# Performance work log

Measured on AMD Instinct MI355X. Metric: run time of the kernel, lower is better.

Reference implementation:

```python
import jax, jax.numpy as jnp
import numpy as np

H = 1024        # hidden_size
NH = 16         # num_attention_heads
DH = H // NH    # head dim = 64
I = 4096        # intermediate_size
E = 8           # moe_num_experts
B, S = 2, 2048
EPS = 1e-12


def _ln(x, g, b):
    mu = jnp.mean(x, axis=-1, keepdims=True)
    var = jnp.mean(jnp.square(x - mu), axis=-1, keepdims=True)
    return (x - mu) * jax.lax.rsqrt(var + EPS) * g + b


def setup_inputs() -> dict:
    key = jax.random.key(0)
    ks = jax.random.split(key, 16)
    std = 0.02
    p = {
        "hidden_states": jax.random.normal(ks[0], (B, S, H), jnp.float32),
        "Wq": jax.random.normal(ks[1], (H, H), jnp.float32) * std,
        "bq": jnp.zeros((H,), jnp.float32),
        "Wk": jax.random.normal(ks[2], (H, H), jnp.float32) * std,
        "bk": jnp.zeros((H,), jnp.float32),
        "Wv": jax.random.normal(ks[3], (H, H), jnp.float32) * std,
        "bv": jnp.zeros((H,), jnp.float32),
        "Wao": jax.random.normal(ks[4], (H, H), jnp.float32) * std,
        "bao": jnp.zeros((H,), jnp.float32),
        "ln1_g": jnp.ones((H,), jnp.float32),
        "ln1_b": jnp.zeros((H,), jnp.float32),
        "router_w": jax.random.normal(ks[5], (H, E), jnp.float32) * std,
        "We": jax.random.normal(ks[6], (E, H, I), jnp.float32) * std,
        "be": jnp.zeros((E, I), jnp.float32),
        "Wo": jax.random.normal(ks[7], (I, H), jnp.float32) * std,
        "bo": jnp.zeros((H,), jnp.float32),
        "ln2_g": jnp.ones((H,), jnp.float32),
        "ln2_b": jnp.zeros((H,), jnp.float32),
    }
    return p


def reference(hidden_states, Wq, bq, Wk, bk, Wv, bv, Wao, bao, ln1_g, ln1_b,
              router_w, We, be, Wo, bo, ln2_g, ln2_b):
    x = hidden_states  # [B,S,H]

    def heads(t):  # [B,S,H] -> [B,NH,S,DH]
        return t.reshape(B, S, NH, DH).transpose(0, 2, 1, 3)

    q = heads(x @ Wq + bq)
    k = heads(x @ Wk + bk)
    v = heads(x @ Wv + bv)
    scores = jnp.einsum("bhqd,bhkd->bhqk", q, k) / jnp.sqrt(jnp.float32(DH))
    probs = jax.nn.softmax(scores, axis=-1)
    ctx = jnp.einsum("bhqk,bhkd->bhqd", probs, v)
    ctx = ctx.transpose(0, 2, 1, 3).reshape(B, S, H)
    attn_out = _ln(ctx @ Wao + bao + x, ln1_g, ln1_b)  # BertSelfOutput

    # ---- MoE FFN: top-1 routing, per-expert GELU MLP, shared output proj ----
    flat = attn_out.reshape(-1, H)              # [N,H]
    logits = flat @ router_w                    # [N,E]
    idx = jnp.argmax(logits, axis=-1)           # top-1 of softmax == argmax of logits
    inter = jnp.zeros((flat.shape[0], I), flat.dtype)
    for e in range(E):  # small fixed expert count
        h_e = jax.nn.gelu(flat @ We[e] + be[e], approximate=False)
        inter = jnp.where((idx == e)[:, None], h_e, inter)
    inter = inter.reshape(B, S, I)
    out = _ln(inter @ Wo + bo + attn_out, ln2_g, ln2_b)  # BertOutput
    return out
```

## Files before the change

### kernel.cpp

```cpp
#include <hip/hip_runtime.h>
#include <hip/hip_bf16.h>
#include <cstdint>

#define H_  1024
#define NH_ 16
#define DH_ 64
#define I_  4096
#define E_  8
#define B_  2
#define S_  2048
#define N_  4096
#define QKVLD 3072
#define LN_EPS 1e-12f

typedef __attribute__((ext_vector_type(4))) float f4;
typedef __attribute__((ext_vector_type(8))) short s8v;
typedef unsigned int u32;

__device__ __forceinline__ float bf2f(unsigned short u) {
  union { unsigned int i; float f; } c; c.i = ((unsigned int)u) << 16; return c.f;
}
__device__ __forceinline__ unsigned short f2bf(float f) {
  __hip_bfloat16 h = __float2bfloat16(f);
  return *reinterpret_cast<unsigned short*>(&h);
}
__device__ __forceinline__ u32 pack_bf2(float a, float b) {
  return (u32)f2bf(a) | ((u32)f2bf(b) << 16);
}
__device__ __forceinline__ float gelu_f(float x) {
  return 0.5f * x * (1.0f + erff(x * 0.70710678118f));
}
__device__ __forceinline__ void gload16(const void* g, void* l) {
  __builtin_amdgcn_global_load_lds(
      (const __attribute__((address_space(1))) void*)g,
      (__attribute__((address_space(3))) void*)l, 16, 0, 0);
}

__global__ __launch_bounds__(256) void cvt_bf16_kernel(
    const float* __restrict__ in, ushort* __restrict__ out, int n8)
{
  const int t = blockIdx.x * 256 + threadIdx.x;
  if (t >= n8) return;
  const f4 x0 = *(const f4*)(in + (size_t)t * 8);
  const f4 x1 = *(const f4*)(in + (size_t)t * 8 + 4);
  s8v o;
#pragma unroll
  for (int j = 0; j < 4; ++j) { o[j] = (short)f2bf(x0[j]); o[4 + j] = (short)f2bf(x1[j]); }
  *(s8v*)(out + (size_t)t * 8) = o;
}

__global__ __launch_bounds__(256) void transpose_cvt_kernel(
    const float* __restrict__ in, ushort* __restrict__ out, int R, int C)
{
  __shared__ float Ls[64][68];
  const size_t zo = (size_t)blockIdx.z * (size_t)R * C;
  const int bx = blockIdx.x << 6;
  const int by = blockIdx.y << 6;
  const int tid = threadIdx.x;
  const int lr = tid >> 4, lc4 = (tid & 15) << 2;
  const float* ip = in + zo + (size_t)(by + lr) * C + bx + lc4;
#pragma unroll
  for (int i = 0; i < 4; ++i)
    *(f4*)&Ls[lr + (i << 4)][lc4] = *(const f4*)(ip + (size_t)(i << 4) * C);
  __syncthreads();
  const int oc = tid >> 2, seg = (tid & 3) << 4;
  ushort* op = out + zo + (size_t)(bx + oc) * R + by + seg;
  s8v v0, v1;
#pragma unroll
  for (int j = 0; j < 8; ++j) {
    v0[j] = (short)f2bf(Ls[seg + j][oc]);
    v1[j] = (short)f2bf(Ls[seg + 8 + j][oc]);
  }
  *(s8v*)op = v0;
  *(s8v*)(op + 8) = v1;
}

__global__ void concat3_kernel(const float* a, const float* b, const float* c,
                               float* __restrict__ o)
{
  const int t = blockIdx.x * 256 + threadIdx.x;
  if (t < 1024) o[t] = a[t];
  else if (t < 2048) o[t] = b[t - 1024];
  else o[t] = c[t - 2048];
}

__global__ __launch_bounds__(256) void gather_kernel(
    const ushort* __restrict__ X, const int* __restrict__ lists,
    ushort* __restrict__ Xg)
{
  const int r = (blockIdx.x << 1) + (threadIdx.x >> 7);
  const int c = (threadIdx.x & 127) << 3;
  const int tok = lists[r];
  *(s8v*)&Xg[(size_t)r * H_ + c] = *(const s8v*)&X[(size_t)tok * H_ + c];
}

__global__ __launch_bounds__(512, 2) void gemm256_bf16_kernel(
    const ushort* __restrict__ A, const ushort* __restrict__ Bt,
    const float* __restrict__ bias, ushort* __restrict__ Cout,
    const int M, const int N, const int K)
{
  __shared__ __align__(16) ushort Asm[2][4][256][8];
  __shared__ __align__(16) ushort Bsm[2][4][256][8];
  const int tid = threadIdx.x, w = tid >> 6, l = tid & 63;
  const int lq = l & 15, g = l >> 4;
  const int wm = w >> 2, wn = w & 3;
  const int nbx = N >> 8;
  const int nwg = nbx * (M >> 8);
  int id = blockIdx.y * nbx + blockIdx.x;
  id = (id & 7) * (nwg >> 3) + (id >> 3);
  const int m0 = (id / nbx) << 8, n0 = (id % nbx) << 8;

  const bool isB = (w >= 4);
  const int ks = w & 3;
  const ushort* gb = isB ? (Bt + (size_t)(n0 + l) * K + (ks << 3))
                         : (A + (size_t)(m0 + l) * K + (ks << 3));
  const ushort* p0 = gb;
  const ushort* p1 = gb + (size_t)64 * K;
  const ushort* p2 = gb + (size_t)128 * K;
  const ushort* p3 = gb + (size_t)192 * K;

  f4 acc[8][4] = {};
  const int nt = K >> 5;
#define STG(tt, buf) { const int kt_ = (tt) << 5;                          \
    ushort* d = isB ? &Bsm[buf][ks][0][0] : &Asm[buf][ks][0][0];           \
    gload16(p0 + kt_, d);          gload16(p1 + kt_, d + 64 * 8);          \
    gload16(p2 + kt_, d + 128 * 8); gload16(p3 + kt_, d + 192 * 8); }
  STG(0, 0);
  STG(1, 1);
  for (int t = 0; t < nt; ++t) {
    const int cur = t & 1;
    if (t + 1 < nt) { asm volatile("s_waitcnt vmcnt(4)" ::: "memory"); }
    else            { asm volatile("s_waitcnt vmcnt(0)" ::: "memory"); }
    __builtin_amdgcn_s_barrier();
    __builtin_amdgcn_sched_barrier(0);
    s8v af[8], bfv[4];
#pragma unroll
    for (int mi = 0; mi < 8; ++mi)
      af[mi] = *(const s8v*)&Asm[cur][g][(wm << 7) + (mi << 4) + lq][0];
#pragma unroll
    for (int ni = 0; ni < 4; ++ni)
      bfv[ni] = *(const s8v*)&Bsm[cur][g][(wn << 6) + (ni << 4) + lq][0];
    asm volatile("s_waitcnt lgkmcnt(0)" ::: "memory");
    __builtin_amdgcn_sched_barrier(0);
    __builtin_amdgcn_s_barrier();
    __builtin_amdgcn_sched_barrier(0);
    if (t + 2 < nt) STG(t + 2, cur);
#pragma unroll
    for (int mi = 0; mi < 8; ++mi)
#pragma unroll
      for (int ni = 0; ni < 4; ++ni)
        acc[mi][ni] = __builtin_amdgcn_mfma_f32_16x16x32_bf16(af[mi], bfv[ni], acc[mi][ni], 0, 0, 0);
  }
#undef STG
  __syncthreads();
  ushort* st = (ushort*)Asm + (size_t)w * (16 * 72);
  float bs[4];
#pragma unroll
  for (int ni = 0; ni < 4; ++ni) bs[ni] = bias[n0 + (wn << 6) + (ni << 4) + lq];
#pragma unroll
  for (int mi = 0; mi < 8; ++mi) {
#pragma unroll
    for (int ni = 0; ni < 4; ++ni)
#pragma unroll
      for (int r = 0; r < 4; ++r)
        st[((g << 2) + r) * 72 + (ni << 4) + lq] = f2bf(acc[mi][ni][r] + bs[ni]);
#pragma unroll
    for (int q2 = 0; q2 < 2; ++q2) {
      const int r16 = l & 15, ch = (l >> 4) + (q2 << 2);
      const s8v vv = *(const s8v*)&st[r16 * 72 + (ch << 3)];
      *(s8v*)&Cout[(size_t)(m0 + (wm << 7) + (mi << 4) + r16) * N
                   + n0 + (wn << 6) + (ch << 3)] = vv;
    }
  }
}

__global__ __launch_bounds__(512, 2) void moe256_mfma_kernel(
    const ushort* __restrict__ Xg, const ushort* __restrict__ WeT,
    const float* __restrict__ be, const int* __restrict__ lists,
    const int* __restrict__ offs, const int* __restrict__ cnt,
    const int* __restrict__ tb, ushort* __restrict__ inter)
{
  __shared__ __align__(16) ushort Asm[2][4][256][8];
  __shared__ __align__(16) ushort Bsm[2][4][256][8];
  __shared__ int tokL[256];
  const int by = blockIdx.y;
  if (by >= tb[E_]) return;
  int e = 0;
#pragma unroll
  for (int t = 1; t < E_; ++t) if (by >= tb[t]) e = t;
  const int rt = by - tb[e];
  const int base = offs[e] + (rt << 8);
  const int nrows = cnt[e] - (rt << 8);
  const int tid = threadIdx.x;
  if (tid < 256) tokL[tid] = (tid < nrows) ? lists[base + tid] : -1;
  __syncthreads();
  const int w = tid >> 6, l = tid & 63;
  const int lq = l & 15, g = l >> 4;
  const int wm = w >> 2, wn = w & 3;
  const int n0 = blockIdx.x << 8;

  const bool isB = (w >= 4);
  const int ks = w & 3;
  const ushort* Wp = WeT + (size_t)e * I_ * H_;
  const ushort* p0;
  const ushort* p1;
  const ushort* p2;
  const ushort* p3;
  if (isB) {
    const ushort* gb = Wp + (size_t)(n0 + l) * H_ + (ks << 3);
    p0 = gb; p1 = gb + (size_t)64 * H_; p2 = gb + (size_t)128 * H_; p3 = gb + (size_t)192 * H_;
  } else {
    p0 = Xg + (size_t)min(base + l,       N_ - 1) * H_ + (ks << 3);
    p1 = Xg + (size_t)min(base + 64 + l,  N_ - 1) * H_ + (ks << 3);
    p2 = Xg + (size_t)min(base + 128 + l, N_ - 1) * H_ + (ks << 3);
    p3 = Xg + (size_t)min(base + 192 + l, N_ - 1) * H_ + (ks << 3);
  }

  f4 acc[8][4] = {};
#define STG(tt, buf) { const int kt_ = (tt) << 5;                          \
    ushort* d = isB ? &Bsm[buf][ks][0][0] : &Asm[buf][ks][0][0];           \
    gload16(p0 + kt_, d);          gload16(p1 + kt_, d + 64 * 8);          \
    gload16(p2 + kt_, d + 128 * 8); gload16(p3 + kt_, d + 192 * 8); }
  STG(0, 0);
  STG(1, 1);
  for (int t = 0; t < 32; ++t) {
    const int cur = t & 1;
    if (t + 1 < 32) { asm volatile("s_waitcnt vmcnt(4)" ::: "memory"); }
    else            { asm volatile("s_waitcnt vmcnt(0)" ::: "memory"); }
    __builtin_amdgcn_s_barrier();
    __builtin_amdgcn_sched_barrier(0);
    s8v af[8], bfv[4];
#pragma unroll
    for (int mi = 0; mi < 8; ++mi)
      af[mi] = *(const s8v*)&Asm[cur][g][(wm << 7) + (mi << 4) + lq][0];
#pragma unroll
    for (int ni = 0; ni < 4; ++ni)
      bfv[ni] = *(const s8v*)&Bsm[cur][g][(wn << 6) + (ni << 4) + lq][0];
    asm volatile("s_waitcnt lgkmcnt(0)" ::: "memory");
    __builtin_amdgcn_sched_barrier(0);
    __builtin_amdgcn_s_barrier();
    __builtin_amdgcn_sched_barrier(0);
    if (t + 2 < 32) STG(t + 2, cur);
#pragma unroll
    for (int mi = 0; mi < 8; ++mi)
#pragma unroll
      for (int ni = 0; ni < 4; ++ni)
        acc[mi][ni] = __builtin_amdgcn_mfma_f32_16x16x32_bf16(af[mi], bfv[ni], acc[mi][ni], 0, 0, 0);
  }
#undef STG
  __syncthreads();
  ushort* st = (ushort*)Asm + (size_t)w * (16 * 72);
  float bs[4];
#pragma unroll
  for (int ni = 0; ni < 4; ++ni)
    bs[ni] = be[(size_t)e * I_ + n0 + (wn << 6) + (ni << 4) + lq];
#pragma unroll
  for (int mi = 0; mi < 8; ++mi) {
#pragma unroll
    for (int ni = 0; ni < 4; ++ni)
#pragma unroll
      for (int r = 0; r < 4; ++r)
        st[((g << 2) + r) * 72 + (ni << 4) + lq] = f2bf(gelu_f(acc[mi][ni][r] + bs[ni]));
#pragma unroll
    for (int q2 = 0; q2 < 2; ++q2) {
      const int r16 = l & 15, ch = (l >> 4) + (q2 << 2);
      const int tok = tokL[(wm << 7) + (mi << 4) + r16];
      if (tok >= 0) {
        const s8v vv = *(const s8v*)&st[r16 * 72 + (ch << 3)];
        *(s8v*)&inter[(size_t)tok * I_ + n0 + (wn << 6) + (ch << 3)] = vv;
      }
    }
  }
}

template <bool BF16OUT, int KSPLIT>
__global__ __launch_bounds__(256, 3) void gemm_mfma_kernel(
    const ushort* __restrict__ A, const ushort* __restrict__ Bt,
    const float* __restrict__ bias, void* __restrict__ Cout,
    const int M, const int N, const int K)
{
  __shared__ __align__(16) ushort Asm[3][4][128][8];
  __shared__ __align__(16) ushort Bsm[3][4][128][8];
  const int tid = threadIdx.x;
  const int w = tid >> 6, l = tid & 63;
  const int lq = l & 15, g = l >> 4;
  const int wm = w >> 1, wn = w & 1;
  const int nbx = N >> 7;
  const int nwg = nbx * (M >> 7);
  int id = blockIdx.y * nbx + blockIdx.x;
  id = (id & 7) * (nwg >> 3) + (id >> 3);
  const int m0 = (id / nbx) << 7, n0 = (id % nbx) << 7;
  const int Kspan = K / KSPLIT;
  const int kbase = (KSPLIT > 1) ? blockIdx.z * Kspan : 0;

  const ushort* a0 = A + (size_t)(m0 + l) * K + kbase + (w << 3);
  const ushort* a1 = a0 + (size_t)64 * K;
  const ushort* b0 = Bt + (size_t)(n0 + l) * K + kbase + (w << 3);
  const ushort* b1 = b0 + (size_t)64 * K;

  f4 acc[4][4] = {};
  const int nt = Kspan >> 5;
#define STAGE_G(tt, buf)                                   \
  { const int kt_ = (tt) << 5;                             \
    gload16(a0 + kt_, &Asm[buf][w][0][0]);                 \
    gload16(a1 + kt_, &Asm[buf][w][64][0]);                \
    gload16(b0 + kt_, &Bsm[buf][w][0][0]);                 \
    gload16(b1 + kt_, &Bsm[buf][w][64][0]); }
  STAGE_G(0, 0);
  STAGE_G(1, 1);
  int cur = 0, nxt2 = 2;
  for (int t = 0; t < nt; ++t) {
    if (t + 1 < nt) { asm volatile("s_waitcnt vmcnt(4)" ::: "memory"); }
    else            { asm volatile("s_waitcnt vmcnt(0)" ::: "memory"); }
    __builtin_amdgcn_s_barrier();
    __builtin_amdgcn_sched_barrier(0);
    if (t + 2 < nt) STAGE_G(t + 2, nxt2);
    s8v af[4], bfv[4];
#pragma unroll
    for (int mi = 0; mi < 4; ++mi)
      af[mi] = *(const s8v*)&Asm[cur][g][(wm << 6) + (mi << 4) + lq][0];
#pragma unroll
    for (int ni = 0; ni < 4; ++ni)
      bfv[ni] = *(const s8v*)&Bsm[cur][g][(wn << 6) + (ni << 4) + lq][0];
    asm volatile("s_waitcnt lgkmcnt(0)" ::: "memory");
    __builtin_amdgcn_sched_barrier(0);
#pragma unroll
    for (int mi = 0; mi < 4; ++mi)
#pragma unroll
      for (int ni = 0; ni < 4; ++ni)
        acc[mi][ni] = __builtin_amdgcn_mfma_f32_16x16x32_bf16(af[mi], bfv[ni], acc[mi][ni], 0, 0, 0);
    cur = (cur == 2) ? 0 : cur + 1;
    nxt2 = (nxt2 == 2) ? 0 : nxt2 + 1;
  }
#undef STAGE_G
  if constexpr (BF16OUT) {
    __syncthreads();
    ushort* st = (ushort*)Asm + (size_t)w * (16 * 72);
    float bs[4];
#pragma unroll
    for (int ni = 0; ni < 4; ++ni) bs[ni] = bias[n0 + (wn << 6) + (ni << 4) + lq];
#pragma unroll
    for (int mi = 0; mi < 4; ++mi) {
#pragma unroll
      for (int ni = 0; ni < 4; ++ni)
#pragma unroll
        for (int r = 0; r < 4; ++r)
          st[((g << 2) + r) * 72 + (ni << 4) + lq] = f2bf(acc[mi][ni][r] + bs[ni]);
#pragma unroll
      for (int q2 = 0; q2 < 2; ++q2) {
        const int r16 = l & 15, ch = (l >> 4) + (q2 << 2);
        const s8v vv = *(const s8v*)&st[r16 * 72 + (ch << 3)];
        *(s8v*)&((ushort*)Cout)[(size_t)(m0 + (wm << 6) + (mi << 4) + r16) * N
                                + n0 + (wn << 6) + (ch << 3)] = vv;
      }
    }
  } else {
    float* outf = (float*)Cout + (size_t)blockIdx.z * M * N;
#pragma unroll
    for (int ni = 0; ni < 4; ++ni) {
      const int col = n0 + (wn << 6) + (ni << 4) + lq;
      const float bs = (KSPLIT == 1 || blockIdx.z == 0) ? bias[col] : 0.f;
#pragma unroll
      for (int mi = 0; mi < 4; ++mi) {
        const int row = m0 + (wm << 6) + (mi << 4) + (g << 2);
#pragma unroll
        for (int r = 0; r < 4; ++r)
          outf[(size_t)(row + r) * N + col] = acc[mi][ni][r] + bs;
      }
    }
  }
}

__global__ __launch_bounds__(256) void attn_mfma_kernel(
    const ushort* __restrict__ qkv, ushort* __restrict__ ctx)
{
  __shared__ __align__(16) ushort Ks[64 * 72];
  __shared__ __align__(16) ushort Vr[64 * 72];
  __shared__ __align__(16) ushort Vt[64 * 72];
  __shared__ __align__(16) ushort Ps[4][16 * 72];
  const int bid0 = blockIdx.x;
  const int bid  = ((bid0 & 7) << 7) + (bid0 >> 3);
  const int bh = bid >> 5, qt = bid & 31;
  const int b = bh >> 4, h = bh & 15;
  const int tid = threadIdx.x, w = tid >> 6, l = tid & 63;
  const int lq = l & 15, g = l >> 4;
  const size_t bS = (size_t)b * S_;
  const ushort* qb = qkv + bS * QKVLD + h * DH_;
  const ushort* kb = qb + 1024;
  const ushort* vb = qb + 2048;

  s8v qf0, qf1;
  {
    const ushort* qp = qb + (size_t)(qt * 64 + w * 16 + lq) * QKVLD;
    qf0 = *(const s8v*)(qp + (g << 3));
    qf1 = *(const s8v*)(qp + 32 + (g << 3));
  }

  f4 o0 = {0,0,0,0}, o1 = {0,0,0,0}, o2 = {0,0,0,0}, o3 = {0,0,0,0};
  float mrun = -3.0e38f, lrun = 0.f;

  const int skey = tid >> 2;
  const int sd   = (tid & 3) << 4;

  s8v kr0, kr1, vr0, vr1;
#define ALOAD(t_) {                                                        \
    const ushort* kp_ = kb + (size_t)((t_) * 64 + skey) * QKVLD + sd;      \
    kr0 = *(const s8v*)kp_; kr1 = *(const s8v*)(kp_ + 8);                  \
    const ushort* vp_ = vb + (size_t)((t_) * 64 + skey) * QKVLD + sd;      \
    vr0 = *(const s8v*)vp_; vr1 = *(const s8v*)(vp_ + 8); }
#define AWRITE() {                                                         \
    *(s8v*)&Ks[skey * 72 + sd]     = kr0;                                  \
    *(s8v*)&Ks[skey * 72 + sd + 8] = kr1;                                  \
    *(s8v*)&Vr[skey * 72 + sd]     = vr0;                                  \
    *(s8v*)&Vr[skey * 72 + sd + 8] = vr1; }

  ALOAD(0); AWRITE();
  ALOAD(1);

  for (int kt = 0; kt < 32; ++kt) {
    asm volatile("s_waitcnt lgkmcnt(0)" ::: "memory");
    __builtin_amdgcn_sched_barrier(0);
    __builtin_amdgcn_s_barrier();
    __builtin_amdgcn_sched_barrier(0);

    {
      s8v t0, t1;
#pragma unroll
      for (int j = 0; j < 8; ++j) {
        t0[j] = (short)Vr[(w * 16 + j) * 72 + l];
        t1[j] = (short)Vr[(w * 16 + 8 + j) * 72 + l];
      }
      *(s8v*)&Vt[l * 72 + w * 16]     = t0;
      *(s8v*)&Vt[l * 72 + w * 16 + 8] = t1;
    }

    float s[16];
    __builtin_amdgcn_s_setprio(1);
#pragma unroll
    for (int st = 0; st < 4; ++st) {
      f4 acc = {0, 0, 0, 0};
      const s8v ka0 = *(const s8v*)&Ks[(st * 16 + lq) * 72 + (g << 3)];
      const s8v ka1 = *(const s8v*)&Ks[(st * 16 + lq) * 72 + 32 + (g << 3)];
      acc = __builtin_amdgcn_mfma_f32_16x16x32_bf16(ka0, qf0, acc, 0, 0, 0);
      acc = __builtin_amdgcn_mfma_f32_16x16x32_bf16(ka1, qf1, acc, 0, 0, 0);
      s[st * 4 + 0] = acc[0] * 0.125f; s[st * 4 + 1] = acc[1] * 0.125f;
      s[st * 4 + 2] = acc[2] * 0.125f; s[st * 4 + 3] = acc[3] * 0.125f;
    }
    __builtin_amdgcn_s_setprio(0);

    float tmax = s[0];
#pragma unroll
    for (int i = 1; i < 16; ++i) tmax = fmaxf(tmax, s[i]);
    tmax = fmaxf(tmax, __shfl_xor(tmax, 16));
    tmax = fmaxf(tmax, __shfl_xor(tmax, 32));
    if (!__all(tmax - mrun <= 8.f)) {
      const float mnew  = fmaxf(mrun, tmax);
      const float alpha = __expf(mrun - mnew);
      f4 av;
      av[0] = __shfl(alpha, g * 4 + 0); av[1] = __shfl(alpha, g * 4 + 1);
      av[2] = __shfl(alpha, g * 4 + 2); av[3] = __shfl(alpha, g * 4 + 3);
      o0 *= av; o1 *= av; o2 *= av; o3 *= av;
      lrun *= alpha; mrun = mnew;
    }
    float psum = 0.f;
#pragma unroll
    for (int i = 0; i < 16; ++i) { s[i] = __expf(s[i] - mrun); psum += s[i]; }
    psum += __shfl_xor(psum, 16); psum += __shfl_xor(psum, 32);
    lrun += psum;

    {
      ushort* pw = &Ps[w][lq * 72];
#pragma unroll
      for (int st = 0; st < 4; ++st) {
        *(u32*)&pw[st * 16 + g * 4 + 0] = pack_bf2(s[st * 4 + 0], s[st * 4 + 1]);
        *(u32*)&pw[st * 16 + g * 4 + 2] = pack_bf2(s[st * 4 + 2], s[st * 4 + 3]);
      }
    }
    asm volatile("s_waitcnt lgkmcnt(0)" ::: "memory");
    __builtin_amdgcn_sched_barrier(0);
    __builtin_amdgcn_s_barrier();
    __builtin_amdgcn_sched_barrier(0);

    __builtin_amdgcn_s_setprio(1);
#pragma unroll
    for (int ks = 0; ks < 2; ++ks) {
      const int kof = ks * 32 + (g << 3);
      const s8v pa = *(const s8v*)&Ps[w][lq * 72 + kof];
      const s8v v0 = *(const s8v*)&Vt[( 0 + lq) * 72 + kof];
      const s8v v1 = *(const s8v*)&Vt[(16 + lq) * 72 + kof];
      const s8v v2 = *(const s8v*)&Vt[(32 + lq) * 72 + kof];
      const s8v v3 = *(const s8v*)&Vt[(48 + lq) * 72 + kof];
      o0 = __builtin_amdgcn_mfma_f32_16x16x32_bf16(pa, v0, o0, 0, 0, 0);
      o1 = __builtin_amdgcn_mfma_f32_16x16x32_bf16(pa, v1, o1, 0, 0, 0);
      o2 = __builtin_amdgcn_mfma_f32_16x16x32_bf16(pa, v2, o2, 0, 0, 0);
      o3 = __builtin_amdgcn_mfma_f32_16x16x32_bf16(pa, v3, o3, 0, 0, 0);
    }
    __builtin_amdgcn_s_setprio(0);

    if (kt + 1 < 32) AWRITE();
    if (kt + 2 < 32) ALOAD(kt + 2);
  }
#undef ALOAD
#undef AWRITE

  const float inv = 1.f / lrun;
#pragma unroll
  for (int r = 0; r < 4; ++r) {
    const float li = __shfl(inv, g * 4 + r);
    ushort* op = ctx + (bS + (size_t)(qt * 64 + w * 16 + g * 4 + r)) * H_ + h * DH_ + lq;
    op[0]  = f2bf(o0[r] * li);
    op[16] = f2bf(o1[r] * li);
    op[32] = f2bf(o2[r] * li);
    op[48] = f2bf(o3[r] * li);
  }
}

template <int P>
__global__ __launch_bounds__(256) void add_ln_kernel(
    const float* __restrict__ a, const float* __restrict__ r,
    const float* __restrict__ g, const float* __restrict__ bta,
    float* __restrict__ out, ushort* __restrict__ ob)
{
  const int row = blockIdx.x, tid = threadIdx.x;
  const size_t base = (size_t)row * H_;
  const float4 xr = *(const float4*)(r + base + (tid << 2));
  float4 x = xr;
#pragma unroll
  for (int pp = 0; pp < P; ++pp) {
    const float4 xa = *(const float4*)(a + (size_t)pp * N_ * H_ + base + (tid << 2));
    x.x += xa.x; x.y += xa.y; x.z += xa.z; x.w += xa.w;
  }
  float s  = x.x + x.y + x.z + x.w;
  float ss = x.x * x.x + x.y * x.y + x.z * x.z + x.w * x.w;
#pragma unroll
  for (int off = 1; off < 64; off <<= 1) { s += __shfl_xor(s, off); ss += __shfl_xor(ss, off); }
  __shared__ float red[8];
  const int w = tid >> 6, ln = tid & 63;
  if (ln == 0) { red[w] = s; red[4 + w] = ss; }
  __syncthreads();
  const float S  = red[0] + red[1] + red[2] + red[3];
  const float SS = red[4] + red[5] + red[6] + red[7];
  const float mu  = S * (1.f / 1024.f);
  const float var = fmaxf(SS * (1.f / 1024.f) - mu * mu, 0.f);
  const float inv = rsqrtf(var + LN_EPS);
  const float4 gg = *(const float4*)&g[tid << 2];
  const float4 bb = *(const float4*)&bta[tid << 2];
  float4 y;
  y.x = (x.x - mu) * inv * gg.x + bb.x;
  y.y = (x.y - mu) * inv * gg.y + bb.y;
  y.z = (x.z - mu) * inv * gg.z + bb.z;
  y.w = (x.w - mu) * inv * gg.w + bb.w;
  *(float4*)&out[base + (tid << 2)] = y;
  if (ob) {
    ushort4 u;
    u.x = f2bf(y.x); u.y = f2bf(y.y); u.z = f2bf(y.z); u.w = f2bf(y.w);
    *(ushort4*)&ob[base + (tid << 2)] = u;
  }
}

__global__ __launch_bounds__(64) void router_kernel(
    const float* __restrict__ x, const float* __restrict__ rw,
    int* __restrict__ idx, int* __restrict__ cnt)
{
  const int t = blockIdx.x, lane = threadIdx.x;
  float acc[8] = {0.f};
  for (int c = 0; c < H_; c += 64) {
    const float xv = x[(size_t)t * H_ + c + lane];
    const float* wr = rw + (size_t)(c + lane) * E_;
    const float4 w0 = *(const float4*)wr;
    const float4 w1 = *(const float4*)(wr + 4);
    acc[0] += xv * w0.x; acc[1] += xv * w0.y; acc[2] += xv * w0.z; acc[3] += xv * w0.w;
    acc[4] += xv * w1.x; acc[5] += xv * w1.y; acc[6] += xv * w1.z; acc[7] += xv * w1.w;
  }
#pragma unroll
  for (int e = 0; e < E_; ++e) {
    float s = acc[e];
#pragma unroll
    for (int off = 1; off < 64; off <<= 1) s += __shfl_xor(s, off);
    acc[e] = s;
  }
  if (lane == 0) {
    int be_ = 0; float bv = acc[0];
#pragma unroll
    for (int e = 1; e < E_; ++e) if (acc[e] > bv) { bv = acc[e]; be_ = e; }
    idx[t] = be_;
    atomicAdd(&cnt[be_], 1);
  }
}

__global__ void init_kernel(int* cnt) { if (threadIdx.x < E_) cnt[threadIdx.x] = 0; }

__global__ void scan_kernel(const int* __restrict__ cnt, int* __restrict__ offs,
                            int* __restrict__ cursor, int* __restrict__ tb)
{
  int o = 0, tt = 0;
  for (int e = 0; e < E_; ++e) {
    offs[e] = o; cursor[e] = o; tb[e] = tt;
    o += cnt[e]; tt += (cnt[e] + 255) >> 8;
  }
  tb[E_] = tt;
}

__global__ __launch_bounds__(256) void scatter_kernel(
    const int* __restrict__ idx, int* __restrict__ cursor, int* __restrict__ lists)
{
  const int t = blockIdx.x * 256 + threadIdx.x;
  if (t < N_) {
    const int e = idx[t];
    const int p = atomicAdd(&cursor[e], 1);
    lists[p] = t;
  }
}

extern "C" void kernel_launch(void* const* d_in, const int* in_sizes, int n_in,
                              void* d_out, int out_size, void* d_ws, size_t ws_size,
                              hipStream_t stream) {
  const float* x   = (const float*)d_in[0];
  const float* Wq  = (const float*)d_in[1];
  const float* bq  = (const float*)d_in[2];
  const float* Wk  = (const float*)d_in[3];
  const float* bk  = (const float*)d_in[4];
  const float* Wv  = (const float*)d_in[5];
  const float* bv  = (const float*)d_in[6];
  const float* Wao = (const float*)d_in[7];
  const float* bao = (const float*)d_in[8];
  const float* g1  = (const float*)d_in[9];
  const float* b1  = (const float*)d_in[10];
  const float* rw  = (const float*)d_in[11];
  const float* We  = (const float*)d_in[12];
  const float* be  = (const float*)d_in[13];
  const float* Wo  = (const float*)d_in[14];
  const float* bo  = (const float*)d_in[15];
  const float* g2  = (const float*)d_in[16];
  const float* b2  = (const float*)d_in[17];
  float* out = (float*)d_out;

  char* p = (char*)d_ws;
  int* idx    = (int*)p; p += (size_t)N_ * 4;
  int* cnt    = (int*)p; p += 8 * 4;
  int* offs   = (int*)p; p += 8 * 4;
  int* cursor = (int*)p; p += 8 * 4;
  int* tb     = (int*)p; p += 16 * 4;
  int* lists  = (int*)p; p += (size_t)N_ * 4;
  p = (char*)(((uintptr_t)p + 255) & ~(uintptr_t)255);
  const size_t NH = (size_t)N_ * H_;
  ushort* xb     = (ushort*)p; p += NH * 2;
  ushort* qkvb   = (ushort*)p;
  float*  woPart = (float*)p;  p += (size_t)N_ * QKVLD * 2;
  ushort* ctxb   = (ushort*)p; p += NH * 2;
  float*  attn   = (float*)p;  p += NH * 4;
  ushort* attnb  = (ushort*)p; p += NH * 2;
  ushort* interb = (ushort*)p;
  float*  aoPart = (float*)p;  p += (size_t)N_ * I_ * 2;
  ushort* WqkvT  = (ushort*)p; p += (size_t)QKVLD * H_ * 2;
  ushort* WaoT   = (ushort*)p; p += (size_t)H_ * H_ * 2;
  ushort* WoT    = (ushort*)p; p += (size_t)H_ * I_ * 2;
  ushort* WeT    = (ushort*)p; p += (size_t)E_ * I_ * H_ * 2;
  float*  bqkv   = (float*)p;  p += QKVLD * 4;
  ushort* Xg     = xb;

  const dim3 blk(256);

  init_kernel<<<1, 64, 0, stream>>>(cnt);
  cvt_bf16_kernel<<<(N_ * H_ / 8 + 255) / 256, blk, 0, stream>>>(x, xb, N_ * H_ / 8);
  concat3_kernel<<<QKVLD / 256, blk, 0, stream>>>(bq, bk, bv, bqkv);
  transpose_cvt_kernel<<<dim3(16, 16, 1), blk, 0, stream>>>(Wq, WqkvT, H_, H_);
  transpose_cvt_kernel<<<dim3(16, 16, 1), blk, 0, stream>>>(Wk, WqkvT + (size_t)1024 * H_, H_, H_);
  transpose_cvt_kernel<<<dim3(16, 16, 1), blk, 0, stream>>>(Wv, WqkvT + (size_t)2048 * H_, H_, H_);
  transpose_cvt_kernel<<<dim3(16, 16, 1), blk, 0, stream>>>(Wao, WaoT, H_, H_);
  transpose_cvt_kernel<<<dim3(16, 64, 1), blk, 0, stream>>>(Wo, WoT, I_, H_);
  transpose_cvt_kernel<<<dim3(64, 16, 8), blk, 0, stream>>>(We, WeT, H_, I_);

  gemm256_bf16_kernel<<<dim3(QKVLD / 256, N_ / 256), dim3(512), 0, stream>>>(
      xb, WqkvT, bqkv, qkvb, N_, QKVLD, H_);
  attn_mfma_kernel<<<1024, blk, 0, stream>>>(qkvb, ctxb);
  gemm_mfma_kernel<false, 2><<<dim3(H_ / 128, N_ / 128, 2), blk, 0, stream>>>(
      ctxb, WaoT, bao, aoPart, N_, H_, H_);
  add_ln_kernel<2><<<N_, blk, 0, stream>>>(aoPart, x, g1, b1, attn, attnb);
  router_kernel<<<N_, 64, 0, stream>>>(attn, rw, idx, cnt);
  scan_kernel<<<1, 1, 0, stream>>>(cnt, offs, cursor, tb);
  scatter_kernel<<<N_ / 256, blk, 0, stream>>>(idx, cursor, lists);
  gather_kernel<<<N_ / 2, blk, 0, stream>>>(attnb, lists, Xg);
  moe256_mfma_kernel<<<dim3(I_ / 256, N_ / 256 + E_), dim3(512), 0, stream>>>(
      Xg, WeT, be, lists, offs, cnt, tb, interb);
  gemm_mfma_kernel<false, 2><<<dim3(H_ / 128, N_ / 128, 2), blk, 0, stream>>>(
      interb, WoT, bo, woPart, N_, H_, I_);
  add_ln_kernel<2><<<N_, blk, 0, stream>>>(woPart, attn, g2, b2, out, (ushort*)nullptr);
}
```

Baseline: 516.6 us.

## Use 256-tile split-K GEMM for projections and fuse routing scan/scatter

Generalizes the 256x256 tile, 512-thread GEMM with a bf16/fp32 output template and a split-K template, and uses it for the attention-output and FFN-output projections instead of the 128x128 kernel. It also folds the expert-count reset into the input conversion kernel and merges the scan and scatter into one single-block kernel with a shared-memory cursor. The intent is higher per-block data reuse and fewer kernel launches. The trade-off is that the projection GEMMs now launch only 128 blocks, which may leave many compute units idle.

```diff
diff --git a/kernel.cpp b/kernel.cpp
--- a/kernel.cpp
+++ b/kernel.cpp
@@ -37,8 +37,9 @@
 }
 
 __global__ __launch_bounds__(256) void cvt_bf16_kernel(
-    const float* __restrict__ in, ushort* __restrict__ out, int n8)
-{
+    const float* __restrict__ in, ushort* __restrict__ out, int n8, int* __restrict__ cnt)
+{
+  if (blockIdx.x == 0 && threadIdx.x < E_) cnt[threadIdx.x] = 0;
   const int t = blockIdx.x * 256 + threadIdx.x;
   if (t >= n8) return;
   const f4 x0 = *(const f4*)(in + (size_t)t * 8);
@@ -84,6 +85,28 @@
   else o[t] = c[t - 2048];
 }
 
+__global__ __launch_bounds__(256) void scan_scatter_kernel(
+    const int* __restrict__ idx, const int* __restrict__ cnt,
+    int* __restrict__ offs, int* __restrict__ tb, int* __restrict__ lists)
+{
+  __shared__ int lcur[E_];
+  const int tid = threadIdx.x;
+  if (tid == 0) {
+    int o = 0, tt = 0;
+    for (int e = 0; e < E_; ++e) {
+      offs[e] = o; lcur[e] = o; tb[e] = tt;
+      o += cnt[e]; tt += (cnt[e] + 255) >> 8;
+    }
+    tb[E_] = tt;
+  }
+  __syncthreads();
+  for (int t = tid; t < N_; t += 256) {
+    const int e = idx[t];
+    const int p = atomicAdd(&lcur[e], 1);
+    lists[p] = t;
+  }
+}
+
 __global__ __launch_bounds__(256) void gather_kernel(
     const ushort* __restrict__ X, const int* __restrict__ lists,
     ushort* __restrict__ Xg)
@@ -94,9 +117,10 @@
   *(s8v*)&Xg[(size_t)r * H_ + c] = *(const s8v*)&X[(size_t)tok * H_ + c];
 }
 
-__global__ __launch_bounds__(512, 2) void gemm256_bf16_kernel(
+template <bool BF16OUT, int KSPLIT>
+__global__ __launch_bounds__(512, 2) void gemm256_kernel(
     const ushort* __restrict__ A, const ushort* __restrict__ Bt,
-    const float* __restrict__ bias, ushort* __restrict__ Cout,
+    const float* __restrict__ bias, void* __restrict__ Cout,
     const int M, const int N, const int K)
 {
   __shared__ __align__(16) ushort Asm[2][4][256][8];
@@ -109,18 +133,20 @@
   int id = blockIdx.y * nbx + blockIdx.x;
   id = (id & 7) * (nwg >> 3) + (id >> 3);
   const int m0 = (id / nbx) << 8, n0 = (id % nbx) << 8;
+  const int Kspan = K / KSPLIT;
+  const int kbase = (KSPLIT > 1) ? blockIdx.z * Kspan : 0;
 
   const bool isB = (w >= 4);
   const int ks = w & 3;
-  const ushort* gb = isB ? (Bt + (size_t)(n0 + l) * K + (ks << 3))
-                         : (A + (size_t)(m0 + l) * K + (ks << 3));
+  const ushort* gb = isB ? (Bt + (size_t)(n0 + l) * K + kbase + (ks << 3))
+                         : (A + (size_t)(m0 + l) * K + kbase + (ks << 3));
   const ushort* p0 = gb;
   const ushort* p1 = gb + (size_t)64 * K;
   const ushort* p2 = gb + (size_t)128 * K;
   const ushort* p3 = gb + (size_t)192 * K;
 
   f4 acc[8][4] = {};
-  const int nt = K >> 5;
+  const int nt = Kspan >> 5;
 #define STG(tt, buf) { const int kt_ = (tt) << 5;                          \
     ushort* d = isB ? &Bsm[buf][ks][0][0] : &Asm[buf][ks][0][0];           \
     gload16(p0 + kt_, d);          gload16(p1 + kt_, d + 64 * 8);          \
@@ -152,24 +178,40 @@
         acc[mi][ni] = __builtin_amdgcn_mfma_f32_16x16x32_bf16(af[mi], bfv[ni], acc[mi][ni], 0, 0, 0);
   }
 #undef STG
-  __syncthreads();
-  ushort* st = (ushort*)Asm + (size_t)w * (16 * 72);
-  float bs[4];
-#pragma unroll
-  for (int ni = 0; ni < 4; ++ni) bs[ni] = bias[n0 + (wn << 6) + (ni << 4) + lq];
-#pragma unroll
-  for (int mi = 0; mi < 8; ++mi) {
-#pragma unroll
-    for (int ni = 0; ni < 4; ++ni)
-#pragma unroll
-      for (int r = 0; r < 4; ++r)
-        st[((g << 2) + r) * 72 + (ni << 4) + lq] = f2bf(acc[mi][ni][r] + bs[ni]);
-#pragma unroll
-    for (int q2 = 0; q2 < 2; ++q2) {
-      const int r16 = l & 15, ch = (l >> 4) + (q2 << 2);
-      const s8v vv = *(const s8v*)&st[r16 * 72 + (ch << 3)];
-      *(s8v*)&Cout[(size_t)(m0 + (wm << 7) + (mi << 4) + r16) * N
-                   + n0 + (wn << 6) + (ch << 3)] = vv;
+  if constexpr (BF16OUT) {
+    __syncthreads();
+    ushort* st = (ushort*)Asm + (size_t)w * (16 * 72);
+    float bs[4];
+#pragma unroll
+    for (int ni = 0; ni < 4; ++ni) bs[ni] = bias[n0 + (wn << 6) + (ni << 4) + lq];
+#pragma unroll
+    for (int mi = 0; mi < 8; ++mi) {
+#pragma unroll
+      for (int ni = 0; ni < 4; ++ni)
+#pragma unroll
+        for (int r = 0; r < 4; ++r)
+          st[((g << 2) + r) * 72 + (ni << 4) + lq] = f2bf(acc[mi][ni][r] + bs[ni]);
+#pragma unroll
+      for (int q2 = 0; q2 < 2; ++q2) {
+        const int r16 = l & 15, ch = (l >> 4) + (q2 << 2);
+        const s8v vv = *(const s8v*)&st[r16 * 72 + (ch << 3)];
+        *(s8v*)&((ushort*)Cout)[(size_t)(m0 + (wm << 7) + (mi << 4) + r16) * N
+                                + n0 + (wn << 6) + (ch << 3)] = vv;
+      }
+    }
+  } else {
+    float* outf = (float*)Cout + (size_t)blockIdx.z * M * N;
+#pragma unroll
+    for (int ni = 0; ni < 4; ++ni) {
+      const int col = n0 + (wn << 6) + (ni << 4) + lq;
+      const float bs = (KSPLIT == 1 || blockIdx.z == 0) ? bias[col] : 0.f;
+#pragma unroll
+      for (int mi = 0; mi < 8; ++mi) {
+        const int row = m0 + (wm << 7) + (mi << 4) + (g << 2);
+#pragma unroll
+        for (int r = 0; r < 4; ++r)
+          outf[(size_t)(row + r) * N + col] = acc[mi][ni][r] + bs;
+      }
     }
   }
 }
@@ -268,104 +310,6 @@
       if (tok >= 0) {
         const s8v vv = *(const s8v*)&st[r16 * 72 + (ch << 3)];
         *(s8v*)&inter[(size_t)tok * I_ + n0 + (wn << 6) + (ch << 3)] = vv;
-      }
-    }
-  }
-}
-
-template <bool BF16OUT, int KSPLIT>
-__global__ __launch_bounds__(256, 3) void gemm_mfma_kernel(
-    const ushort* __restrict__ A, const ushort* __restrict__ Bt,
-    const float* __restrict__ bias, void* __restrict__ Cout,
-    const int M, const int N, const int K)
-{
-  __shared__ __align__(16) ushort Asm[3][4][128][8];
-  __shared__ __align__(16) ushort Bsm[3][4][128][8];
-  const int tid = threadIdx.x;
-  const int w = tid >> 6, l = tid & 63;
-  const int lq = l & 15, g = l >> 4;
-  const int wm = w >> 1, wn = w & 1;
-  const int nbx = N >> 7;
-  const int nwg = nbx * (M >> 7);
-  int id = blockIdx.y * nbx + blockIdx.x;
-  id = (id & 7) * (nwg >> 3) + (id >> 3);
-  const int m0 = (id / nbx) << 7, n0 = (id % nbx) << 7;
-  const int Kspan = K / KSPLIT;
-  const int kbase = (KSPLIT > 1) ? blockIdx.z * Kspan : 0;
-
-  const ushort* a0 = A + (size_t)(m0 + l) * K + kbase + (w << 3);
-  const ushort* a1 = a0 + (size_t)64 * K;
-  const ushort* b0 = Bt + (size_t)(n0 + l) * K + kbase + (w << 3);
-  const ushort* b1 = b0 + (size_t)64 * K;
-
-  f4 acc[4][4] = {};
-  const int nt = Kspan >> 5;
-#define STAGE_G(tt, buf)                                   \
-  { const int kt_ = (tt) << 5;                             \
-    gload16(a0 + kt_, &Asm[buf][w][0][0]);                 \
-    gload16(a1 + kt_, &Asm[buf][w][64][0]);                \
-    gload16(b0 + kt_, &Bsm[buf][w][0][0]);                 \
-    gload16(b1 + kt_, &Bsm[buf][w][64][0]); }
-  STAGE_G(0, 0);
-  STAGE_G(1, 1);
-  int cur = 0, nxt2 = 2;
-  for (int t = 0; t < nt; ++t) {
-    if (t + 1 < nt) { asm volatile("s_waitcnt vmcnt(4)" ::: "memory"); }
-    else            { asm volatile("s_waitcnt vmcnt(0)" ::: "memory"); }
-    __builtin_amdgcn_s_barrier();
-    __builtin_amdgcn_sched_barrier(0);
-    if (t + 2 < nt) STAGE_G(t + 2, nxt2);
-    s8v af[4], bfv[4];
-#pragma unroll
-    for (int mi = 0; mi < 4; ++mi)
-      af[mi] = *(const s8v*)&Asm[cur][g][(wm << 6) + (mi << 4) + lq][0];
-#pragma unroll
-    for (int ni = 0; ni < 4; ++ni)
-      bfv[ni] = *(const s8v*)&Bsm[cur][g][(wn << 6) + (ni << 4) + lq][0];
-    asm volatile("s_waitcnt lgkmcnt(0)" ::: "memory");
-    __builtin_amdgcn_sched_barrier(0);
-#pragma unroll
-    for (int mi = 0; mi < 4; ++mi)
-#pragma unroll
-      for (int ni = 0; ni < 4; ++ni)
-        acc[mi][ni] = __builtin_amdgcn_mfma_f32_16x16x32_bf16(af[mi], bfv[ni], acc[mi][ni], 0, 0, 0);
-    cur = (cur == 2) ? 0 : cur + 1;
-    nxt2 = (nxt2 == 2) ? 0 : nxt2 + 1;
-  }
-#undef STAGE_G
-  if constexpr (BF16OUT) {
-    __syncthreads();
-    ushort* st = (ushort*)Asm + (size_t)w * (16 * 72);
-    float bs[4];
-#pragma unroll
-    for (int ni = 0; ni < 4; ++ni) bs[ni] = bias[n0 + (wn << 6) + (ni << 4) + lq];
-#pragma unroll
-    for (int mi = 0; mi < 4; ++mi) {
-#pragma unroll
-      for (int ni = 0; ni < 4; ++ni)
-#pragma unroll
-        for (int r = 0; r < 4; ++r)
-          st[((g << 2) + r) * 72 + (ni << 4) + lq] = f2bf(acc[mi][ni][r] + bs[ni]);
-#pragma unroll
-      for (int q2 = 0; q2 < 2; ++q2) {
-        const int r16 = l & 15, ch = (l >> 4) + (q2 << 2);
-        const s8v vv = *(const s8v*)&st[r16 * 72 + (ch << 3)];
-        *(s8v*)&((ushort*)Cout)[(size_t)(m0 + (wm << 6) + (mi << 4) + r16) * N
-                                + n0 + (wn << 6) + (ch << 3)] = vv;
-      }
-    }
-  } else {
-    float* outf = (float*)Cout + (size_t)blockIdx.z * M * N;
-#pragma unroll
-    for (int ni = 0; ni < 4; ++ni) {
-      const int col = n0 + (wn << 6) + (ni << 4) + lq;
-      const float bs = (KSPLIT == 1 || blockIdx.z == 0) ? bias[col] : 0.f;
-#pragma unroll
-      for (int mi = 0; mi < 4; ++mi) {
-        const int row = m0 + (wm << 6) + (mi << 4) + (g << 2);
-#pragma unroll
-        for (int r = 0; r < 4; ++r)
-          outf[(size_t)(row + r) * N + col] = acc[mi][ni][r] + bs;
       }
     }
   }
@@ -588,30 +532,6 @@
   }
 }
 
-__global__ void init_kernel(int* cnt) { if (threadIdx.x < E_) cnt[threadIdx.x] = 0; }
-
-__global__ void scan_kernel(const int* __restrict__ cnt, int* __restrict__ offs,
-                            int* __restrict__ cursor, int* __restrict__ tb)
-{
-  int o = 0, tt = 0;
-  for (int e = 0; e < E_; ++e) {
-    offs[e] = o; cursor[e] = o; tb[e] = tt;
-    o += cnt[e]; tt += (cnt[e] + 255) >> 8;
-  }
-  tb[E_] = tt;
-}
-
-__global__ __launch_bounds__(256) void scatter_kernel(
-    const int* __restrict__ idx, int* __restrict__ cursor, int* __restrict__ lists)
-{
-  const int t = blockIdx.x * 256 + threadIdx.x;
-  if (t < N_) {
-    const int e = idx[t];
-    const int p = atomicAdd(&cursor[e], 1);
-    lists[p] = t;
-  }
-}
-
 extern "C" void kernel_launch(void* const* d_in, const int* in_sizes, int n_in,
                               void* d_out, int out_size, void* d_ws, size_t ws_size,
                               hipStream_t stream) {
@@ -639,7 +559,6 @@
   int* idx    = (int*)p; p += (size_t)N_ * 4;
   int* cnt    = (int*)p; p += 8 * 4;
   int* offs   = (int*)p; p += 8 * 4;
-  int* cursor = (int*)p; p += 8 * 4;
   int* tb     = (int*)p; p += 16 * 4;
   int* lists  = (int*)p; p += (size_t)N_ * 4;
   p = (char*)(((uintptr_t)p + 255) & ~(uintptr_t)255);
@@ -660,9 +579,9 @@
   ushort* Xg     = xb;
 
   const dim3 blk(256);
-
-  init_kernel<<<1, 64, 0, stream>>>(cnt);
-  cvt_bf16_kernel<<<(N_ * H_ / 8 + 255) / 256, blk, 0, stream>>>(x, xb, N_ * H_ / 8);
+  const dim3 blk512(512);
+
+  cvt_bf16_kernel<<<(N_ * H_ / 8 + 255) / 256, blk, 0, stream>>>(x, xb, N_ * H_ / 8, cnt);
   concat3_kernel<<<QKVLD / 256, blk, 0, stream>>>(bq, bk, bv, bqkv);
   transpose_cvt_kernel<<<dim3(16, 16, 1), blk, 0, stream>>>(Wq, WqkvT, H_, H_);
   transpose_cvt_kernel<<<dim3(16, 16, 1), blk, 0, stream>>>(Wk, WqkvT + (size_t)1024 * H_, H_, H_);
@@ -671,19 +590,18 @@
   transpose_cvt_kernel<<<dim3(16, 64, 1), blk, 0, stream>>>(Wo, WoT, I_, H_);
   transpose_cvt_kernel<<<dim3(64, 16, 8), blk, 0, stream>>>(We, WeT, H_, I_);
 
-  gemm256_bf16_kernel<<<dim3(QKVLD / 256, N_ / 256), dim3(512), 0, stream>>>(
+  gemm256_kernel<true, 1><<<dim3(QKVLD / 256, N_ / 256), blk512, 0, stream>>>(
       xb, WqkvT, bqkv, qkvb, N_, QKVLD, H_);
   attn_mfma_kernel<<<1024, blk, 0, stream>>>(qkvb, ctxb);
-  gemm_mfma_kernel<false, 2><<<dim3(H_ / 128, N_ / 128, 2), blk, 0, stream>>>(
+  gemm256_kernel<false, 2><<<dim3(H_ / 256, N_ / 256, 2), blk512, 0, stream>>>(
       ctxb, WaoT, bao, aoPart, N_, H_, H_);
   add_ln_kernel<2><<<N_, blk, 0, stream>>>(aoPart, x, g1, b1, attn, attnb);
   router_kernel<<<N_, 64, 0, stream>>>(attn, rw, idx, cnt);
-  scan_kernel<<<1, 1, 0, stream>>>(cnt, offs, cursor, tb);
-  scatter_kernel<<<N_ / 256, blk, 0, stream>>>(idx, cursor, lists);
+  scan_scatter_kernel<<<1, blk, 0, stream>>>(idx, cnt, offs, tb, lists);
   gather_kernel<<<N_ / 2, blk, 0, stream>>>(attnb, lists, Xg);
-  moe256_mfma_kernel<<<dim3(I_ / 256, N_ / 256 + E_), dim3(512), 0, stream>>>(
+  moe256_mfma_kernel<<<dim3(I_ / 256, N_ / 256 + E_), blk512, 0, stream>>>(
       Xg, WeT, be, lists, offs, cnt, tb, interb);
-  gemm_mfma_kernel<false, 2><<<dim3(H_ / 128, N_ / 128, 2), blk, 0, stream>>>(
+  gemm256_kernel<false, 2><<<dim3(H_ / 256, N_ / 256, 2), blk512, 0, stream>>>(
       interb, WoT, bo, woPart, N_, H_, I_);
   add_ln_kernel<2><<<N_, blk, 0, stream>>>(woPart, attn, g2, b2, out, (ushort*)nullptr);
 }
```

After: 507.3 us. No clear change (-1.8%).
